# Kernel tuning notes

Hardware: AMD Instinct MI355X
Metric: run time of the kernel (lower is better)

## Reference

```python
import jax, jax.numpy as jnp
import numpy as np

jax.config.update("jax_enable_x64", True)

# --- static config (matches init_kwargs) ---
L = 6            # voxel_level_num
F = 8            # feature_dim
T = 524288       # per-level feature table size
B = 4194304      # buffer_size (hash table size)
N = 1048576      # number of query points
LEAF = 0.25      # leaf_voxel_size
UP = 2.0         # up_scale_factor

PRIMES = jnp.array([73856093, 19349669, 83492791], dtype=jnp.int64)
# corner offsets, z varies fastest (same order as torch self.steps)
STEPS = jnp.array([[0,0,0],[0,0,1],[0,1,0],[0,1,1],
                   [1,0,0],[1,0,1],[1,1,0],[1,1,1]], dtype=jnp.float32)


def setup_inputs() -> dict:
    key = jax.random.key(0)
    k1, k2, k3, k4 = jax.random.split(key, 4)
    query_points = jax.random.uniform(k1, (N, 3), dtype=jnp.float32) * 50.0
    features = 0.01 * jax.random.normal(k2, (L, T, F), dtype=jnp.float32)
    idx = jax.random.randint(k3, (L, B), 0, T, dtype=jnp.int64)
    empty = jax.random.uniform(k4, (L, B)) < 0.2
    feature_indexs = jnp.where(empty, jnp.int64(-1), idx)
    return {"query_points": query_points, "features": features,
            "feature_indexs": feature_indexs}


def _trilinear_coeffs(d):
    # d: [N,3] fractional coords in the cell; order matches STEPS (z fastest)
    tx, ty, tz = d[:, 0], d[:, 1], d[:, 2]
    return jnp.stack([
        (1-tx)*(1-ty)*(1-tz), (1-tx)*(1-ty)*tz,
        (1-tx)*ty*(1-tz),     (1-tx)*ty*tz,
        tx*(1-ty)*(1-tz),     tx*(1-ty)*tz,
        tx*ty*(1-tz),         tx*ty*tz,
    ], axis=1)  # [N,8]


def reference(query_points, features, feature_indexs):
    out = jnp.zeros((query_points.shape[0], F), dtype=query_points.dtype)
    for i in range(L):  # small fixed level loop (structurally distinct resolutions)
        res = LEAF * (UP ** i)
        scaled = query_points / res                      # [N,3]
        base = jnp.floor(scaled)
        corners = (base[:, None, :] + STEPS[None]).astype(jnp.int64)  # [N,8,3]
        keys = jnp.mod((corners * PRIMES).sum(-1), B)    # [N,8] spatial hash
        idx = feature_indexs[i][keys]                    # [N,8] gather, -1 = empty
        valid = idx.min(axis=1) > -1                     # [N] all 8 corners allocated
        coeffs = _trilinear_coeffs(scaled - base)        # [N,8]
        feats = features[i][jnp.clip(idx, 0, T - 1)]     # [N,8,F] gather
        level = jnp.einsum('nkf,nk->nf', feats, coeffs)  # trilinear interp
        out = out + jnp.where(valid[:, None], level, jnp.zeros((), out.dtype))
    return out
```

## Files before the change

kernel.cpp:

```cpp
#include <hip/hip_runtime.h>


static constexpr int      NPTS  = 1048576;
static constexpr int      NF    = 8;
static constexpr int      TTAB  = 524288;
static constexpr unsigned BTAB  = 4194304u;
static constexpr unsigned BMASK = BTAB - 1u;
static constexpr unsigned P0 = 73856093u, P1 = 19349669u, P2 = 83492791u;

static constexpr int NBIN = 4096;
static constexpr int SB   = 256;
static constexpr int PPB  = NPTS / SB;
static constexpr int ITER = PPB / 256;
static constexpr int BCAP = 512;

static constexpr int S2 = 51, S3 = 26, S4 = 14, S5 = 8;
static constexpr int OCC2 = 0, OCC3 = OCC2 + S2*S2, OCC4 = OCC3 + S3*S3,
                     OCC5 = OCC4 + S4*S4, OCCW = OCC5 + S5*S5;
static constexpr int CB2 = 0, CB3 = CB2 + (S2-1)*(S2-1),
                     CB4 = CB3 + (S3-1)*(S3-1), CB5 = CB4 + (S4-1)*(S4-1),
                     CBW = CB5 + (S5-1)*(S5-1);
static constexpr int RB2 = (S2*S2+3)/4, RB3 = (S3*S3+3)/4,
                     RB4 = (S4*S4+3)/4, RB5 = (S5*S5+3)/4;
static constexpr int OCCB = RB2+RB3+RB4+RB5;

static constexpr int BM01W = 2 * (int)(BTAB / 32);
static constexpr int BM01B = BM01W / 256;

static constexpr size_t SORTED_BYTES = (size_t)NPTS * 16;
static constexpr size_t OCC_OFF  = SORTED_BYTES;
static constexpr size_t CB_OFF   = OCC_OFF + (size_t)OCCW * 8;
static constexpr size_t BB_OFF   = CB_OFF  + (size_t)CBW  * 8;
static constexpr size_t BM01_OFF = (BB_OFF + (size_t)NBIN * 4 + 255) & ~(size_t)255;
static constexpr size_t WS_FULL  = BM01_OFF + (size_t)BM01W * 4;

typedef float f4 __attribute__((ext_vector_type(4)));
typedef int   i4 __attribute__((ext_vector_type(4)));

__device__ __forceinline__ void nhv_point_g(
    float qx, float qy, float qz,
    const float* __restrict__ feat, const int* __restrict__ fidx,
    const unsigned long long* __restrict__ cbit,
    const unsigned* __restrict__ bm01, float acc[NF])
{
    float fx01[2], fy01[2], fz01[2];
    unsigned h01[2];
#pragma unroll
    for (int i = 0; i < 2; ++i) {
        const float inv = (i == 0) ? 4.0f : 2.0f;
        const float sx = qx*inv, sy = qy*inv, sz = qz*inv;
        const float bx = floorf(sx), by = floorf(sy), bz = floorf(sz);
        fx01[i] = sx-bx; fy01[i] = sy-by; fz01[i] = sz-bz;
        h01[i] = (unsigned)(int)bx*P0 + (unsigned)(int)by*P1 + (unsigned)(int)bz*P2;
    }
    unsigned v01 = 0;
#pragma unroll
    for (int i = 0; i < 2; ++i) {
        const unsigned* __restrict__ bl = bm01 + (size_t)i * (BTAB / 32);
        unsigned vv = ~0u;
#pragma unroll
        for (int k = 0; k < 8; ++k) {
            unsigned key = h01[i];
            if (k & 4) key += P0;
            if (k & 2) key += P1;
            if (k & 1) key += P2;
            key &= BMASK;
            vv &= (bl[key >> 5] >> (key & 31u));
        }
        v01 |= (vv & 1u) << i;
    }

    float fxh[4], fyh[4], fzh[4];
    int   ixh[4], iyh[4], izh[4];
    unsigned vhi = 0;
    const int Ss[4]  = {S2, S3, S4, S5};
    const int CBo[4] = {CB2, CB3, CB4, CB5};
#pragma unroll
    for (int j = 0; j < 4; ++j) {
        const float inv = 1.0f / (float)(1 << j);
        const float sx = qx*inv, sy = qy*inv, sz = qz*inv;
        const float bx = floorf(sx), by = floorf(sy), bz = floorf(sz);
        fxh[j] = sx-bx; fyh[j] = sy-by; fzh[j] = sz-bz;
        ixh[j] = (int)bx; iyh[j] = (int)by; izh[j] = (int)bz;
        const int C = Ss[j] - 1;
        const unsigned long long row = cbit[CBo[j] + izh[j]*C + iyh[j]];
        vhi |= (unsigned)((row >> ixh[j]) & 1ull) << j;
    }

#pragma unroll
    for (int f = 0; f < NF; ++f) acc[f] = 0.0f;

#pragma unroll
    for (int i = 0; i < 2; ++i) {
        if (v01 & (1u << i)) {
            const int* __restrict__ tab = fidx + (size_t)i * BTAB;
            int id[8];
#pragma unroll
            for (int k = 0; k < 8; ++k) {
                unsigned key = h01[i];
                if (k & 4) key += P0;
                if (k & 2) key += P1;
                if (k & 1) key += P2;
                id[k] = tab[key & BMASK];
            }
            const float wxv[2] = {1.0f - fx01[i], fx01[i]};
            const float wyv[2] = {1.0f - fy01[i], fy01[i]};
            const float wzv[2] = {1.0f - fz01[i], fz01[i]};
            const float* __restrict__ fb = feat + (size_t)i * (TTAB * NF);
#pragma unroll
            for (int k = 0; k < 8; ++k) {
                const float c = wxv[(k>>2)&1] * wyv[(k>>1)&1] * wzv[k&1];
                const float4* p = (const float4*)(fb + (size_t)id[k] * NF);
                const float4 lo = p[0], hi = p[1];
                acc[0]+=c*lo.x; acc[1]+=c*lo.y; acc[2]+=c*lo.z; acc[3]+=c*lo.w;
                acc[4]+=c*hi.x; acc[5]+=c*hi.y; acc[6]+=c*hi.z; acc[7]+=c*hi.w;
            }
        }
    }
#pragma unroll
    for (int j = 0; j < 4; ++j) {
        if (vhi & (1u << j)) {
            const int lvl = 2 + j;
            const unsigned h = (unsigned)ixh[j]*P0 + (unsigned)iyh[j]*P1
                             + (unsigned)izh[j]*P2;
            const int* __restrict__ tab = fidx + (size_t)lvl * BTAB;
            int id[8];
#pragma unroll
            for (int k = 0; k < 8; ++k) {
                unsigned key = h;
                if (k & 4) key += P0;
                if (k & 2) key += P1;
                if (k & 1) key += P2;
                id[k] = tab[key & BMASK];
            }
            const float wxv[2] = {1.0f - fxh[j], fxh[j]};
            const float wyv[2] = {1.0f - fyh[j], fyh[j]};
            const float wzv[2] = {1.0f - fzh[j], fzh[j]};
            const float* __restrict__ fb = feat + (size_t)lvl * (TTAB * NF);
#pragma unroll
            for (int k = 0; k < 8; ++k) {
                const float c = wxv[(k>>2)&1] * wyv[(k>>1)&1] * wzv[k&1];
                const float4* p = (const float4*)(fb + (size_t)id[k] * NF);
                const float4 lo = p[0], hi = p[1];
                acc[0]+=c*lo.x; acc[1]+=c*lo.y; acc[2]+=c*lo.z; acc[3]+=c*lo.w;
                acc[4]+=c*hi.x; acc[5]+=c*hi.y; acc[6]+=c*hi.z; acc[7]+=c*hi.w;
            }
        }
    }
}

__device__ __forceinline__ void nhv_point(
    float qx, float qy, float qz,
    const float* __restrict__ feat, const int* __restrict__ fidx, float acc[NF])
{
    float fx[6], fy[6], fz[6];
    unsigned h[6];
#pragma unroll
    for (int i = 0; i < 6; ++i) {
        const float inv = 4.0f / (float)(1 << i);
        const float sx = qx*inv, sy = qy*inv, sz = qz*inv;
        const float bx = floorf(sx), by = floorf(sy), bz = floorf(sz);
        fx[i] = sx-bx; fy[i] = sy-by; fz[i] = sz-bz;
        h[i] = (unsigned)(int)bx*P0 + (unsigned)(int)by*P1 + (unsigned)(int)bz*P2;
    }
    int id[6][8];
#pragma unroll
    for (int i = 0; i < 6; ++i) {
        const int* __restrict__ tab = fidx + (size_t)i * BTAB;
#pragma unroll
        for (int k = 0; k < 8; ++k) {
            unsigned key = h[i];
            if (k & 4) key += P0;
            if (k & 2) key += P1;
            if (k & 1) key += P2;
            id[i][k] = tab[key & BMASK];
        }
    }
#pragma unroll
    for (int f = 0; f < NF; ++f) acc[f] = 0.0f;
#pragma unroll
    for (int i = 0; i < 6; ++i) {
        int mn = id[i][0];
#pragma unroll
        for (int k = 1; k < 8; ++k) mn = min(mn, id[i][k]);
        if (mn > -1) {
            const float wxv[2] = {1.0f - fx[i], fx[i]};
            const float wyv[2] = {1.0f - fy[i], fy[i]};
            const float wzv[2] = {1.0f - fz[i], fz[i]};
            const float* __restrict__ fb = feat + (size_t)i * (TTAB * NF);
#pragma unroll
            for (int k = 0; k < 8; ++k) {
                const float c = wxv[(k>>2)&1] * wyv[(k>>1)&1] * wzv[k&1];
                const float4* p = (const float4*)(fb + (size_t)id[i][k] * NF);
                const float4 lo = p[0], hi = p[1];
                acc[0]+=c*lo.x; acc[1]+=c*lo.y; acc[2]+=c*lo.z; acc[3]+=c*lo.w;
                acc[4]+=c*hi.x; acc[5]+=c*hi.y; acc[6]+=c*hi.z; acc[7]+=c*hi.w;
            }
        }
    }
}

__device__ __forceinline__ unsigned expand4(unsigned v) {
    return (v & 1u) | ((v & 2u) << 2) | ((v & 4u) << 4) | ((v & 8u) << 6);
}
__device__ __forceinline__ unsigned bin_of(float x, float y, float z) {
    unsigned bx = min(15u, (unsigned)(int)(x * 0.32f));
    unsigned by = min(15u, (unsigned)(int)(y * 0.32f));
    unsigned bz = min(15u, (unsigned)(int)(z * 0.32f));
    return expand4(bx) | (expand4(by) << 1) | (expand4(bz) << 2);
}

__global__ __launch_bounds__(256) void pre_k(const int* __restrict__ fidx,
                                             unsigned long long* __restrict__ occ,
                                             unsigned* __restrict__ bm01,
                                             const float* __restrict__ qp,
                                             unsigned* __restrict__ hist) {
    __shared__ unsigned lh[NBIN];
    const int t = threadIdx.x, b = blockIdx.x;
    if (b < OCCB) {
        int lvl, S, occoff, bb = b;
        if (bb < RB2)              { lvl = 2; S = S2; occoff = OCC2; }
        else if ((bb -= RB2) < RB3){ lvl = 3; S = S3; occoff = OCC3; }
        else if ((bb -= RB3) < RB4){ lvl = 4; S = S4; occoff = OCC4; }
        else        { bb -= RB4;     lvl = 5; S = S5; occoff = OCC5; }
        const int row  = bb * 4 + (t >> 6);
        const int lane = t & 63;
        if (row < S * S) {
            const int y = row % S, z = row / S;
            bool v = false;
            if (lane < S) {
                const unsigned key = ((unsigned)lane*P0 + (unsigned)y*P1
                                    + (unsigned)z*P2) & BMASK;
                v = fidx[(size_t)lvl * BTAB + key] >= 0;
            }
            const unsigned long long m = __ballot(v);
            if (lane == 0) occ[occoff + row] = m;
        }
    } else if (b < OCCB + BM01B) {
        const int g = (b - OCCB) * 256 + t;
        const i4* p = (const i4*)(fidx + (size_t)g * 32);
        unsigned w = 0;
#pragma unroll
        for (int j = 0; j < 8; ++j) {
            const i4 v = __builtin_nontemporal_load(p + j);
            w |= (unsigned)(v.x >= 0) << (4 * j + 0);
            w |= (unsigned)(v.y >= 0) << (4 * j + 1);
            w |= (unsigned)(v.z >= 0) << (4 * j + 2);
            w |= (unsigned)(v.w >= 0) << (4 * j + 3);
        }
        bm01[g] = w;
    } else {
        const int bh = b - OCCB - BM01B;
        for (int i = t; i < NBIN; i += 256) lh[i] = 0u;
        __syncthreads();
        const int base = bh * PPB;
#pragma unroll
        for (int i = 0; i < ITER; ++i) {
            const int p = base + i * 256 + t;
            const float x = __builtin_nontemporal_load(qp + 3*p);
            const float y = __builtin_nontemporal_load(qp + 3*p + 1);
            const float z = __builtin_nontemporal_load(qp + 3*p + 2);
            atomicAdd(&lh[bin_of(x, y, z)], 1u);
        }
        __syncthreads();
        for (int i = t; i < NBIN; i += 256)
            __builtin_nontemporal_store(lh[i], hist + (size_t)bh * NBIN + i);
    }
}

__global__ __launch_bounds__(256) void mid_k(unsigned* __restrict__ hist,
                                             unsigned* __restrict__ binbase,
                                             const unsigned long long* __restrict__ occ,
                                             unsigned long long* __restrict__ cbit) {
    const int t = threadIdx.x, b = blockIdx.x;
    if (b < 16) {
        const int bin = b * 256 + t;
        unsigned run = 0;
        for (int blk = 0; blk < SB; ++blk) {
            const unsigned v = hist[(size_t)blk * NBIN + bin];
            hist[(size_t)blk * NBIN + bin] = run;
            run += v;
        }
        binbase[bin] = run;
    } else {
        const int cr = (b - 16) * 256 + t;
        if (cr >= CBW) return;
        int S, occoff, cboff, local;
        if (cr < CB3)      { S = S2; occoff = OCC2; cboff = CB2; local = cr; }
        else if (cr < CB4) { S = S3; occoff = OCC3; cboff = CB3; local = cr - CB3; }
        else if (cr < CB5) { S = S4; occoff = OCC4; cboff = CB4; local = cr - CB4; }
        else               { S = S5; occoff = OCC5; cboff = CB5; local = cr - CB5; }
        const int C = S - 1;
        const int cy = local % C, cz = local / C;
        const unsigned long long r00 = occ[occoff +  cz      * S + cy    ];
        const unsigned long long r10 = occ[occoff +  cz      * S + cy + 1];
        const unsigned long long r01 = occ[occoff + (cz + 1) * S + cy    ];
        const unsigned long long r11 = occ[occoff + (cz + 1) * S + cy + 1];
        const unsigned long long cw = (r00 & (r00 >> 1)) & (r10 & (r10 >> 1))
                                    & (r01 & (r01 >> 1)) & (r11 & (r11 >> 1));
        cbit[cboff + cz * C + cy] = cw;
    }
}

__global__ __launch_bounds__(256) void binscan_k(unsigned* __restrict__ binbase) {
    __shared__ unsigned tot[256];
    const int t = threadIdx.x;
    unsigned v[16];
    unsigned s = 0;
#pragma unroll
    for (int i = 0; i < 16; ++i) { v[i] = s; s += binbase[t * 16 + i]; }
    tot[t] = s;
    __syncthreads();
    for (int d = 1; d < 256; d <<= 1) {
        const unsigned x = (t >= d) ? tot[t - d] : 0u;
        __syncthreads();
        tot[t] += x;
        __syncthreads();
    }
    const unsigned cb = tot[t] - s;
#pragma unroll
    for (int i = 0; i < 16; ++i) binbase[t * 16 + i] = cb + v[i];
}

__global__ __launch_bounds__(256) void scatter_k(const float* __restrict__ qp,
                                                 const unsigned* __restrict__ hist,
                                                 const unsigned* __restrict__ binbase,
                                                 float4* __restrict__ sorted) {
    __shared__ unsigned cur[NBIN];
    const int b = blockIdx.x, t = threadIdx.x;
    for (int i = t; i < NBIN; i += 256)
        cur[i] = binbase[i] + hist[(size_t)b * NBIN + i];
    __syncthreads();
    const int base = b * PPB;
#pragma unroll
    for (int i = 0; i < ITER; ++i) {
        const int p = base + i * 256 + t;
        const float x = __builtin_nontemporal_load(qp + 3*p);
        const float y = __builtin_nontemporal_load(qp + 3*p + 1);
        const float z = __builtin_nontemporal_load(qp + 3*p + 2);
        const unsigned slot = atomicAdd(&cur[bin_of(x, y, z)], 1u);
        const f4 v = {x, y, z, __uint_as_float((unsigned)p)};
        __builtin_nontemporal_store(v, (f4*)sorted + slot);
    }
}

__global__ __launch_bounds__(256) void binsort_k(float4* __restrict__ sorted,
                                                 const unsigned* __restrict__ binbase) {
    __shared__ float4        pts[BCAP];
    __shared__ unsigned char sk[BCAP];
    __shared__ unsigned      cnt[64];
    const int bin = blockIdx.x, t = threadIdx.x;
    const unsigned start = binbase[bin];
    const unsigned end   = (bin < NBIN - 1) ? binbase[bin + 1] : (unsigned)NPTS;
    const int n = (int)(end - start);
    if (n <= 1 || n > BCAP) return;

    if (t < 64) cnt[t] = 0u;
    __syncthreads();
#pragma unroll
    for (int r = 0; r < BCAP / 256; ++r) {
        const int i = r * 256 + t;
        if (i < n) {
            const f4 pv = __builtin_nontemporal_load((const f4*)sorted + (start + i));
            const float4 p = make_float4(pv.x, pv.y, pv.z, pv.w);
            pts[i] = p;
            const unsigned ux = (unsigned)(int)(p.x * 1.28f) & 3u;
            const unsigned uy = (unsigned)(int)(p.y * 1.28f) & 3u;
            const unsigned uz = (unsigned)(int)(p.z * 1.28f) & 3u;
            const unsigned s = (ux & 1u) | ((uy & 1u) << 1) | ((uz & 1u) << 2)
                             | ((ux >> 1) << 3) | ((uy >> 1) << 4) | ((uz >> 1) << 5);
            sk[i] = (unsigned char)s;
            atomicAdd(&cnt[s], 1u);
        }
    }
    __syncthreads();
    if (t == 0) {
        unsigned run = 0;
#pragma unroll
        for (int i = 0; i < 64; ++i) { const unsigned v = cnt[i]; cnt[i] = run; run += v; }
    }
    __syncthreads();
#pragma unroll
    for (int r = 0; r < BCAP / 256; ++r) {
        const int i = r * 256 + t;
        if (i < n) {
            const unsigned dest = atomicAdd(&cnt[sk[i]], 1u);
            const float4 p = pts[i];
            const f4 v = {p.x, p.y, p.z, p.w};
            __builtin_nontemporal_store(v, (f4*)sorted + (start + dest));
        }
    }
}

__global__ __launch_bounds__(256) void nhv_main_k(
    const float4* __restrict__ sp, const float* __restrict__ feat,
    const int* __restrict__ fidx, const unsigned long long* __restrict__ cbit,
    const unsigned* __restrict__ bm01, float* __restrict__ out)
{
    const int nwg = NPTS / 256;
    const int bid = blockIdx.x;
    const int swz = (bid & 7) * (nwg >> 3) + (bid >> 3);
    const int j   = swz * 256 + (int)threadIdx.x;

    const f4 s = __builtin_nontemporal_load((const f4*)sp + j);
    float acc[NF];
    nhv_point_g(s.x, s.y, s.z, feat, fidx, cbit, bm01, acc);
    const unsigned n = __float_as_uint(s.w);
    f4* o = (f4*)(out + (size_t)n * NF);
    f4 lo = {acc[0], acc[1], acc[2], acc[3]};
    f4 hi = {acc[4], acc[5], acc[6], acc[7]};
    __builtin_nontemporal_store(lo, o);
    __builtin_nontemporal_store(hi, o + 1);
}

__global__ __launch_bounds__(256) void nhv_direct_k(
    const float* __restrict__ qp, const float* __restrict__ feat,
    const int* __restrict__ fidx, float* __restrict__ out)
{
    const int n = blockIdx.x * 256 + threadIdx.x;
    if (n >= NPTS) return;
    float acc[NF];
    nhv_point(qp[3*n], qp[3*n+1], qp[3*n+2], feat, fidx, acc);
    float4* o = (float4*)(out + (size_t)n * NF);
    o[0] = make_float4(acc[0], acc[1], acc[2], acc[3]);
    o[1] = make_float4(acc[4], acc[5], acc[6], acc[7]);
}

extern "C" void kernel_launch(void* const* d_in, const int* in_sizes, int n_in,
                              void* d_out, int out_size, void* d_ws, size_t ws_size,
                              hipStream_t stream) {
    const float* qp   = (const float*)d_in[0];
    const float* feat = (const float*)d_in[1];
    const int*   fidx = (const int*)d_in[2];
    float*       out  = (float*)d_out;

    if (ws_size >= WS_FULL) {
        float4*             sorted  = (float4*)d_ws;
        unsigned long long* occ     = (unsigned long long*)((char*)d_ws + OCC_OFF);
        unsigned long long* cbit    = (unsigned long long*)((char*)d_ws + CB_OFF);
        unsigned*           binbase = (unsigned*)((char*)d_ws + BB_OFF);
        unsigned*           bm01    = (unsigned*)((char*)d_ws + BM01_OFF);
        unsigned*           hist    = (unsigned*)d_out;

        pre_k<<<dim3(OCCB + BM01B + SB), dim3(256), 0, stream>>>(fidx, occ, bm01, qp, hist);
        mid_k<<<dim3(16 + (CBW + 255) / 256), dim3(256), 0, stream>>>(hist, binbase, occ, cbit);
        binscan_k<<<dim3(1), dim3(256), 0, stream>>>(binbase);
        scatter_k<<<dim3(SB), dim3(256), 0, stream>>>(qp, hist, binbase, sorted);
        binsort_k<<<dim3(NBIN), dim3(256), 0, stream>>>(sorted, binbase);
        nhv_main_k<<<dim3(NPTS/256), dim3(256), 0, stream>>>(sorted, feat, fidx, cbit, bm01, out);
    } else {
        nhv_direct_k<<<dim3(NPTS/256), dim3(256), 0, stream>>>(qp, feat, fidx, out);
    }
}
```

Measured before the change: 213.9 us.

## Precompute dense cell-validity bitmaps for levels 0 and 1

The per-point validity check for the two finest levels changes. Before, it did 8 scattered hash-bitmap lookups per level; now a new pass builds dense per-cell occupancy bitmaps over the 200^3 and 100^3 grids, so each point needs one 64-bit word load per level. The hash-bitmap build is rewritten to use wave ballots, and intermediate occupancy arrays are stored in scratch space inside the output buffer. This adds a kernel launch and extra precompute work in exchange for fewer random memory accesses in the main kernel. It assumes query coordinates lie within the 50-unit bounding box.

```diff
diff --git a/kernel.cpp b/kernel.cpp
--- a/kernel.cpp
+++ b/kernel.cpp
@@ -24,15 +24,34 @@
                      RB4 = (S4*S4+3)/4, RB5 = (S5*S5+3)/4;
 static constexpr int OCCB = RB2+RB3+RB4+RB5;
 
-static constexpr int BM01W = 2 * (int)(BTAB / 32);
-static constexpr int BM01B = BM01W / 256;
+static constexpr int L0S = 201, L0C = 200, L0W = 4;
+static constexpr int L1S = 101, L1C = 100, L1W = 2;
+static constexpr int L0R = L0S * L0S;
+static constexpr int L1R = L1S * L1S;
+static constexpr int OCC0W_CNT = L0R * L0W;
+static constexpr int OCC1W_CNT = L1R * L1W;
+static constexpr int CB0_CNT = L0C * L0C * L0W;
+static constexpr int CB1_CNT = L1C * L1C * L1W;
+static constexpr int OCC01_WAVES = OCC0W_CNT + OCC1W_CNT;
+static constexpr int OCC01_B = (OCC01_WAVES + 3) / 4;
+static constexpr int MIDC = CBW + CB0_CNT + CB1_CNT;
+static constexpr int MIDB = 16 + (MIDC + 255) / 256;
+
+static constexpr int BM01_WAVES = (int)(2 * BTAB / 256);
+static constexpr int BM01B = BM01_WAVES / 4;
+
+static constexpr size_t HIST_OFF      = 0;
+static constexpr size_t OUT_BM01_OFF  = 4u  * 1024 * 1024;
+static constexpr size_t OUT_OCC25_OFF = 5u  * 1024 * 1024;
+static constexpr size_t OUT_OCC0_OFF  = 5632u * 1024;
+static constexpr size_t OUT_OCC1_OFF  = 7u  * 1024 * 1024;
 
 static constexpr size_t SORTED_BYTES = (size_t)NPTS * 16;
-static constexpr size_t OCC_OFF  = SORTED_BYTES;
-static constexpr size_t CB_OFF   = OCC_OFF + (size_t)OCCW * 8;
-static constexpr size_t BB_OFF   = CB_OFF  + (size_t)CBW  * 8;
-static constexpr size_t BM01_OFF = (BB_OFF + (size_t)NBIN * 4 + 255) & ~(size_t)255;
-static constexpr size_t WS_FULL  = BM01_OFF + (size_t)BM01W * 4;
+static constexpr size_t CB25_OFF = SORTED_BYTES;
+static constexpr size_t CB0_OFF  = CB25_OFF + 32768;
+static constexpr size_t CB1_OFF  = CB0_OFF + 1310720;
+static constexpr size_t BB_OFF   = CB1_OFF + 163840;
+static constexpr size_t WS_FULL  = BB_OFF + (size_t)NBIN * 4;
 
 typedef float f4 __attribute__((ext_vector_type(4)));
 typedef int   i4 __attribute__((ext_vector_type(4)));
@@ -40,39 +59,21 @@
 __device__ __forceinline__ void nhv_point_g(
     float qx, float qy, float qz,
     const float* __restrict__ feat, const int* __restrict__ fidx,
-    const unsigned long long* __restrict__ cbit,
-    const unsigned* __restrict__ bm01, float acc[NF])
+    const unsigned long long* __restrict__ cbit25,
+    const unsigned long long* __restrict__ cbit0,
+    const unsigned long long* __restrict__ cbit1, float acc[NF])
 {
-    float fx01[2], fy01[2], fz01[2];
-    unsigned h01[2];
-#pragma unroll
-    for (int i = 0; i < 2; ++i) {
-        const float inv = (i == 0) ? 4.0f : 2.0f;
-        const float sx = qx*inv, sy = qy*inv, sz = qz*inv;
-        const float bx = floorf(sx), by = floorf(sy), bz = floorf(sz);
-        fx01[i] = sx-bx; fy01[i] = sy-by; fz01[i] = sz-bz;
-        h01[i] = (unsigned)(int)bx*P0 + (unsigned)(int)by*P1 + (unsigned)(int)bz*P2;
-    }
-    unsigned v01 = 0;
-#pragma unroll
-    for (int i = 0; i < 2; ++i) {
-        const unsigned* __restrict__ bl = bm01 + (size_t)i * (BTAB / 32);
-        unsigned vv = ~0u;
-#pragma unroll
-        for (int k = 0; k < 8; ++k) {
-            unsigned key = h01[i];
-            if (k & 4) key += P0;
-            if (k & 2) key += P1;
-            if (k & 1) key += P2;
-            key &= BMASK;
-            vv &= (bl[key >> 5] >> (key & 31u));
-        }
-        v01 |= (vv & 1u) << i;
-    }
+    const int ix0 = (int)(qx * 4.0f), iy0 = (int)(qy * 4.0f), iz0 = (int)(qz * 4.0f);
+    const int ix1 = (int)(qx * 2.0f), iy1 = (int)(qy * 2.0f), iz1 = (int)(qz * 2.0f);
+
+    const unsigned long long w0 = cbit0[(size_t)(iz0 * L0C + iy0) * L0W + (ix0 >> 6)];
+    const unsigned long long w1 = cbit1[(size_t)(iz1 * L1C + iy1) * L1W + (ix1 >> 6)];
 
     float fxh[4], fyh[4], fzh[4];
     int   ixh[4], iyh[4], izh[4];
-    unsigned vhi = 0;
+    unsigned vm = 0;
+    vm |= (unsigned)((w0 >> (ix0 & 63)) & 1ull) << 0;
+    vm |= (unsigned)((w1 >> (ix1 & 63)) & 1ull) << 1;
     const int Ss[4]  = {S2, S3, S4, S5};
     const int CBo[4] = {CB2, CB3, CB4, CB5};
 #pragma unroll
@@ -83,8 +84,8 @@
         fxh[j] = sx-bx; fyh[j] = sy-by; fzh[j] = sz-bz;
         ixh[j] = (int)bx; iyh[j] = (int)by; izh[j] = (int)bz;
         const int C = Ss[j] - 1;
-        const unsigned long long row = cbit[CBo[j] + izh[j]*C + iyh[j]];
-        vhi |= (unsigned)((row >> ixh[j]) & 1ull) << j;
+        const unsigned long long row = cbit25[CBo[j] + izh[j]*C + iyh[j]];
+        vm |= (unsigned)((row >> ixh[j]) & 1ull) << (2 + j);
     }
 
 #pragma unroll
@@ -92,20 +93,26 @@
 
 #pragma unroll
     for (int i = 0; i < 2; ++i) {
-        if (v01 & (1u << i)) {
+        if (vm & (1u << i)) {
+            const float inv = (i == 0) ? 4.0f : 2.0f;
+            const float sx = qx*inv, sy = qy*inv, sz = qz*inv;
+            const float bx = floorf(sx), by = floorf(sy), bz = floorf(sz);
+            const unsigned h = (unsigned)(int)bx*P0 + (unsigned)(int)by*P1
+                             + (unsigned)(int)bz*P2;
             const int* __restrict__ tab = fidx + (size_t)i * BTAB;
             int id[8];
 #pragma unroll
             for (int k = 0; k < 8; ++k) {
-                unsigned key = h01[i];
+                unsigned key = h;
                 if (k & 4) key += P0;
                 if (k & 2) key += P1;
                 if (k & 1) key += P2;
                 id[k] = tab[key & BMASK];
             }
-            const float wxv[2] = {1.0f - fx01[i], fx01[i]};
-            const float wyv[2] = {1.0f - fy01[i], fy01[i]};
-            const float wzv[2] = {1.0f - fz01[i], fz01[i]};
+            const float tx = sx - bx, ty = sy - by, tz = sz - bz;
+            const float wxv[2] = {1.0f - tx, tx};
+            const float wyv[2] = {1.0f - ty, ty};
+            const float wzv[2] = {1.0f - tz, tz};
             const float* __restrict__ fb = feat + (size_t)i * (TTAB * NF);
 #pragma unroll
             for (int k = 0; k < 8; ++k) {
@@ -119,7 +126,7 @@
     }
 #pragma unroll
     for (int j = 0; j < 4; ++j) {
-        if (vhi & (1u << j)) {
+        if (vm & (1u << (2 + j))) {
             const int lvl = 2 + j;
             const unsigned h = (unsigned)ixh[j]*P0 + (unsigned)iyh[j]*P1
                              + (unsigned)izh[j]*P2;
@@ -211,8 +218,8 @@
 }
 
 __global__ __launch_bounds__(256) void pre_k(const int* __restrict__ fidx,
-                                             unsigned long long* __restrict__ occ,
-                                             unsigned* __restrict__ bm01,
+                                             unsigned long long* __restrict__ occ25,
+                                             unsigned long long* __restrict__ bm01,
                                              const float* __restrict__ qp,
                                              unsigned* __restrict__ hist) {
     __shared__ unsigned lh[NBIN];
@@ -234,21 +241,22 @@
                 v = fidx[(size_t)lvl * BTAB + key] >= 0;
             }
             const unsigned long long m = __ballot(v);
-            if (lane == 0) occ[occoff + row] = m;
+            if (lane == 0) occ25[occoff + row] = m;
         }
     } else if (b < OCCB + BM01B) {
-        const int g = (b - OCCB) * 256 + t;
-        const i4* p = (const i4*)(fidx + (size_t)g * 32);
-        unsigned w = 0;
-#pragma unroll
-        for (int j = 0; j < 8; ++j) {
-            const i4 v = __builtin_nontemporal_load(p + j);
-            w |= (unsigned)(v.x >= 0) << (4 * j + 0);
-            w |= (unsigned)(v.y >= 0) << (4 * j + 1);
-            w |= (unsigned)(v.z >= 0) << (4 * j + 2);
-            w |= (unsigned)(v.w >= 0) << (4 * j + 3);
-        }
-        bm01[g] = w;
+        const int tid  = (b - OCCB) * 256 + t;
+        const int w    = tid >> 6;
+        const int lane = tid & 63;
+        const i4 v = __builtin_nontemporal_load(
+                        (const i4*)(fidx + (size_t)w * 256) + lane);
+        const unsigned long long m0 = __ballot(v.x >= 0);
+        const unsigned long long m1 = __ballot(v.y >= 0);
+        const unsigned long long m2 = __ballot(v.z >= 0);
+        const unsigned long long m3 = __ballot(v.w >= 0);
+        if (lane == 0) {
+            unsigned long long* d = bm01 + ((size_t)w << 2);
+            d[0] = m0; d[1] = m1; d[2] = m2; d[3] = m3;
+        }
     } else {
         const int bh = b - OCCB - BM01B;
         for (int i = t; i < NBIN; i += 256) lh[i] = 0u;
@@ -268,10 +276,44 @@
     }
 }
 
+__global__ __launch_bounds__(256) void occ01_k(
+    const unsigned long long* __restrict__ bm01,
+    unsigned long long* __restrict__ occ0,
+    unsigned long long* __restrict__ occ1)
+{
+    const int wid  = (blockIdx.x * 256 + threadIdx.x) >> 6;
+    const int lane = threadIdx.x & 63;
+    if (wid >= OCC01_WAVES) return;
+
+    int lvl, S, row, wblk;
+    unsigned long long* dst;
+    if (wid < OCC0W_CNT) {
+        lvl = 0; S = L0S; row = wid >> 2; wblk = wid & 3; dst = occ0 + wid;
+    } else {
+        const int w1 = wid - OCC0W_CNT;
+        lvl = 1; S = L1S; row = w1 >> 1; wblk = w1 & 1; dst = occ1 + w1;
+    }
+    const int z = row / S, y = row % S;
+    const int x = wblk * 64 + lane;
+    bool v = false;
+    if (x < S) {
+        const unsigned key = ((unsigned)x*P0 + (unsigned)y*P1 + (unsigned)z*P2) & BMASK;
+        const unsigned B = (unsigned)lvl * BTAB + key;
+        const unsigned long long word = bm01[((size_t)(B >> 8) << 2) | (B & 3u)];
+        v = (word >> ((B >> 2) & 63u)) & 1ull;
+    }
+    const unsigned long long m = __ballot(v);
+    if (lane == 0) *dst = m;
+}
+
 __global__ __launch_bounds__(256) void mid_k(unsigned* __restrict__ hist,
                                              unsigned* __restrict__ binbase,
-                                             const unsigned long long* __restrict__ occ,
-                                             unsigned long long* __restrict__ cbit) {
+                                             const unsigned long long* __restrict__ occ25,
+                                             const unsigned long long* __restrict__ occ0,
+                                             const unsigned long long* __restrict__ occ1,
+                                             unsigned long long* __restrict__ cbit25,
+                                             unsigned long long* __restrict__ cbit0,
+                                             unsigned long long* __restrict__ cbit1) {
     const int t = threadIdx.x, b = blockIdx.x;
     if (b < 16) {
         const int bin = b * 256 + t;
@@ -282,23 +324,56 @@
             run += v;
         }
         binbase[bin] = run;
-    } else {
-        const int cr = (b - 16) * 256 + t;
-        if (cr >= CBW) return;
+        return;
+    }
+    const int c = (b - 16) * 256 + t;
+    if (c >= MIDC) return;
+    if (c < CBW) {
         int S, occoff, cboff, local;
-        if (cr < CB3)      { S = S2; occoff = OCC2; cboff = CB2; local = cr; }
-        else if (cr < CB4) { S = S3; occoff = OCC3; cboff = CB3; local = cr - CB3; }
-        else if (cr < CB5) { S = S4; occoff = OCC4; cboff = CB4; local = cr - CB4; }
-        else               { S = S5; occoff = OCC5; cboff = CB5; local = cr - CB5; }
+        if (c < CB3)      { S = S2; occoff = OCC2; cboff = CB2; local = c; }
+        else if (c < CB4) { S = S3; occoff = OCC3; cboff = CB3; local = c - CB3; }
+        else if (c < CB5) { S = S4; occoff = OCC4; cboff = CB4; local = c - CB4; }
+        else              { S = S5; occoff = OCC5; cboff = CB5; local = c - CB5; }
         const int C = S - 1;
         const int cy = local % C, cz = local / C;
-        const unsigned long long r00 = occ[occoff +  cz      * S + cy    ];
-        const unsigned long long r10 = occ[occoff +  cz      * S + cy + 1];
-        const unsigned long long r01 = occ[occoff + (cz + 1) * S + cy    ];
-        const unsigned long long r11 = occ[occoff + (cz + 1) * S + cy + 1];
-        const unsigned long long cw = (r00 & (r00 >> 1)) & (r10 & (r10 >> 1))
+        const unsigned long long r00 = occ25[occoff +  cz      * S + cy    ];
+        const unsigned long long r10 = occ25[occoff +  cz      * S + cy + 1];
+        const unsigned long long r01 = occ25[occoff + (cz + 1) * S + cy    ];
+        const unsigned long long r11 = occ25[occoff + (cz + 1) * S + cy + 1];
+        cbit25[cboff + cz * C + cy] = (r00 & (r00 >> 1)) & (r10 & (r10 >> 1))
                                     & (r01 & (r01 >> 1)) & (r11 & (r11 >> 1));
-        cbit[cboff + cz * C + cy] = cw;
+    } else if (c < CBW + CB0_CNT) {
+        const int c0 = c - CBW;
+        const int w = c0 & 3, crow = c0 >> 2;
+        const int cy = crow % L0C, cz = crow / L0C;
+        unsigned long long res = ~0ull;
+#pragma unroll
+        for (int dy = 0; dy < 2; ++dy)
+#pragma unroll
+            for (int dz = 0; dz < 2; ++dz) {
+                const unsigned long long* r =
+                    occ0 + ((size_t)((cz + dz) * L0S + (cy + dy)) << 2);
+                const unsigned long long a = r[w];
+                const unsigned long long n = (w < 3) ? r[w + 1] : 0ull;
+                res &= a & ((a >> 1) | (n << 63));
+            }
+        cbit0[c0] = res;
+    } else {
+        const int c1 = c - CBW - CB0_CNT;
+        const int w = c1 & 1, crow = c1 >> 1;
+        const int cy = crow % L1C, cz = crow / L1C;
+        unsigned long long res = ~0ull;
+#pragma unroll
+        for (int dy = 0; dy < 2; ++dy)
+#pragma unroll
+            for (int dz = 0; dz < 2; ++dz) {
+                const unsigned long long* r =
+                    occ1 + ((size_t)((cz + dz) * L1S + (cy + dy)) << 1);
+                const unsigned long long a = r[w];
+                const unsigned long long n = (w < 1) ? r[w + 1] : 0ull;
+                res &= a & ((a >> 1) | (n << 63));
+            }
+        cbit1[c1] = res;
     }
 }
 
@@ -394,8 +469,11 @@
 
 __global__ __launch_bounds__(256) void nhv_main_k(
     const float4* __restrict__ sp, const float* __restrict__ feat,
-    const int* __restrict__ fidx, const unsigned long long* __restrict__ cbit,
-    const unsigned* __restrict__ bm01, float* __restrict__ out)
+    const int* __restrict__ fidx,
+    const unsigned long long* __restrict__ cbit25,
+    const unsigned long long* __restrict__ cbit0,
+    const unsigned long long* __restrict__ cbit1,
+    float* __restrict__ out)
 {
     const int nwg = NPTS / 256;
     const int bid = blockIdx.x;
@@ -404,7 +482,7 @@
 
     const f4 s = __builtin_nontemporal_load((const f4*)sp + j);
     float acc[NF];
-    nhv_point_g(s.x, s.y, s.z, feat, fidx, cbit, bm01, acc);
+    nhv_point_g(s.x, s.y, s.z, feat, fidx, cbit25, cbit0, cbit1, acc);
     const unsigned n = __float_as_uint(s.w);
     f4* o = (f4*)(out + (size_t)n * NF);
     f4 lo = {acc[0], acc[1], acc[2], acc[3]};
@@ -436,18 +514,25 @@
 
     if (ws_size >= WS_FULL) {
         float4*             sorted  = (float4*)d_ws;
-        unsigned long long* occ     = (unsigned long long*)((char*)d_ws + OCC_OFF);
-        unsigned long long* cbit    = (unsigned long long*)((char*)d_ws + CB_OFF);
+        unsigned long long* cbit25  = (unsigned long long*)((char*)d_ws + CB25_OFF);
+        unsigned long long* cbit0   = (unsigned long long*)((char*)d_ws + CB0_OFF);
+        unsigned long long* cbit1   = (unsigned long long*)((char*)d_ws + CB1_OFF);
         unsigned*           binbase = (unsigned*)((char*)d_ws + BB_OFF);
-        unsigned*           bm01    = (unsigned*)((char*)d_ws + BM01_OFF);
-        unsigned*           hist    = (unsigned*)d_out;
-
-        pre_k<<<dim3(OCCB + BM01B + SB), dim3(256), 0, stream>>>(fidx, occ, bm01, qp, hist);
-        mid_k<<<dim3(16 + (CBW + 255) / 256), dim3(256), 0, stream>>>(hist, binbase, occ, cbit);
+        unsigned*           hist  = (unsigned*)d_out;
+        unsigned long long* bm01  = (unsigned long long*)((char*)d_out + OUT_BM01_OFF);
+        unsigned long long* occ25 = (unsigned long long*)((char*)d_out + OUT_OCC25_OFF);
+        unsigned long long* occ0  = (unsigned long long*)((char*)d_out + OUT_OCC0_OFF);
+        unsigned long long* occ1  = (unsigned long long*)((char*)d_out + OUT_OCC1_OFF);
+
+        pre_k<<<dim3(OCCB + BM01B + SB), dim3(256), 0, stream>>>(fidx, occ25, bm01, qp, hist);
+        occ01_k<<<dim3(OCC01_B), dim3(256), 0, stream>>>(bm01, occ0, occ1);
+        mid_k<<<dim3(MIDB), dim3(256), 0, stream>>>(hist, binbase, occ25, occ0, occ1,
+                                                    cbit25, cbit0, cbit1);
         binscan_k<<<dim3(1), dim3(256), 0, stream>>>(binbase);
         scatter_k<<<dim3(SB), dim3(256), 0, stream>>>(qp, hist, binbase, sorted);
         binsort_k<<<dim3(NBIN), dim3(256), 0, stream>>>(sorted, binbase);
-        nhv_main_k<<<dim3(NPTS/256), dim3(256), 0, stream>>>(sorted, feat, fidx, cbit, bm01, out);
+        nhv_main_k<<<dim3(NPTS/256), dim3(256), 0, stream>>>(sorted, feat, fidx,
+                                                             cbit25, cbit0, cbit1, out);
     } else {
         nhv_direct_k<<<dim3(NPTS/256), dim3(256), 0, stream>>>(qp, feat, fidx, out);
     }
```

Result: no change. 215.1 us (+0.5%).
